# Kernel optimization log

Hardware: AMD Instinct MI355X
Metric: run time of the kernel (lower is better)

## Reference

```python
import jax, jax.numpy as jnp
import numpy as np

TOP_K = 2  # num_experts_per_tok


def setup_inputs() -> dict:
    key = jax.random.key(0)
    ks = jax.random.split(key, 5)
    B, T, D, E, F = 2, 2048, 1024, 8, 2048
    scale_d = 1.0 / np.sqrt(D)
    scale_f = 1.0 / np.sqrt(F)
    return {
        "x": jax.random.normal(ks[0], (B, T, D), jnp.float32),
        "kernel_router_DE": jax.random.normal(ks[1], (D, E), jnp.float32) * scale_d,
        "kernel_gating_EDF": jax.random.normal(ks[2], (E, D, F), jnp.float32) * scale_d,
        "kernel_up_EDF": jax.random.normal(ks[3], (E, D, F), jnp.float32) * scale_d,
        "kernel_down_EFD": jax.random.normal(ks[4], (E, F, D), jnp.float32) * scale_f,
    }


def reference(x, kernel_router_DE, kernel_gating_EDF, kernel_up_EDF, kernel_down_EFD):
    E = kernel_router_DE.shape[-1]
    x = x.astype(jnp.float32)

    # --- Router: logits -> softmax -> top_k -> renormalize with softmax ---
    router_logits_BTE = jnp.einsum('BTD,DE->BTE', x, kernel_router_DE)
    probs_BTE = jax.nn.softmax(router_logits_BTE.astype(jnp.float32), axis=-1)
    weights_BTX, indices_BTX = jax.lax.top_k(probs_BTE, TOP_K)
    norm_weights_BTX = jax.nn.softmax(weights_BTX, axis=-1)

    # --- Scatter top-k weights back to dense per-expert weights ---
    one_hot_BTXE = jax.nn.one_hot(indices_BTX, num_classes=E, dtype=jnp.float32)
    full_weights_BTE = jnp.sum(one_hot_BTXE * norm_weights_BTX[..., None], axis=2)

    # --- Dense all-expert MLP (gating * up -> down), weighted combine ---
    gating_BTEF = jnp.einsum('BTD,EDF->BTEF', x, kernel_gating_EDF)
    fuse_BTEF = jax.nn.silu(gating_BTEF) * jnp.einsum('BTD,EDF->BTEF', x, kernel_up_EDF)
    down_BTED = jnp.einsum('BTEF,EFD->BTED', fuse_BTEF, kernel_down_EFD)
    out_BTD = jnp.einsum('BTED,BTE->BTD', down_BTED, full_weights_BTE)
    return out_BTD.astype(jnp.float32)
```

## Files before the change

### kernel.cpp

```cpp
#include <hip/hip_runtime.h>
#include <cstdint>

#define N_TOK 4096
#define DIM   1024
#define NEXP  8
#define FDIM  2048

typedef _Float16 f16_t;
typedef _Float16 f16x8 __attribute__((ext_vector_type(8)));
typedef float    f32x4 __attribute__((ext_vector_type(4)));

__device__ inline unsigned packh(float a, float b) {
    union { f16_t h[2]; unsigned u; } p;
    p.h[0] = (f16_t)a; p.h[1] = (f16_t)b;
    return p.u;
}

__device__ inline void gl2lds16(const void* g, void* l) {
    __builtin_amdgcn_global_load_lds(
        (const __attribute__((address_space(1))) unsigned*)g,
        (__attribute__((address_space(3))) unsigned*)l, 16, 0, 0);
}

template<int N>
__device__ inline void vmw() {
    asm volatile("s_waitcnt vmcnt(%0)" :: "i"(N) : "memory");
}

__global__ __launch_bounds__(256) void router_kernel(
    const float* __restrict__ x, const float* __restrict__ wr,
    float* __restrict__ topw, int* __restrict__ counts, int* __restrict__ bucket)
{
    __shared__ float r[NEXP][DIM];
    __shared__ int sIdx[32];
    int tid = threadIdx.x;
    for (int i = tid; i < DIM * NEXP / 4; i += 256) {
        float4 v = ((const float4*)wr)[i];
        int base = i * 4;
        r[(base + 0) & 7][(base + 0) >> 3] = v.x;
        r[(base + 1) & 7][(base + 1) >> 3] = v.y;
        r[(base + 2) & 7][(base + 2) >> 3] = v.z;
        r[(base + 3) & 7][(base + 3) >> 3] = v.w;
    }
    __syncthreads();
    int wave = tid >> 6, lane = tid & 63;
    int t0 = blockIdx.x * 16 + wave * 4;
    for (int tt = 0; tt < 4; ++tt) {
        int t = t0 + tt;
        float acc[NEXP];
#pragma unroll
        for (int e = 0; e < NEXP; e++) acc[e] = 0.f;
        const float* xr = x + (size_t)t * DIM;
#pragma unroll
        for (int k = 0; k < DIM / 64; k++) {
            int d = lane + k * 64;
            float xv = xr[d];
#pragma unroll
            for (int e = 0; e < NEXP; e++) acc[e] += xv * r[e][d];
        }
#pragma unroll
        for (int e = 0; e < NEXP; e++) {
#pragma unroll
            for (int off = 32; off > 0; off >>= 1)
                acc[e] += __shfl_xor(acc[e], off, 64);
        }
        if (lane == 0) {
            float mx = acc[0];
#pragma unroll
            for (int e = 1; e < NEXP; e++) mx = fmaxf(mx, acc[e]);
            float p[NEXP]; float s = 0.f;
#pragma unroll
            for (int e = 0; e < NEXP; e++) { p[e] = expf(acc[e] - mx); s += p[e]; }
            float inv = 1.f / s;
#pragma unroll
            for (int e = 0; e < NEXP; e++) p[e] *= inv;
            int i1 = 0; float p1 = p[0];
#pragma unroll
            for (int e = 1; e < NEXP; e++) if (p[e] > p1) { p1 = p[e]; i1 = e; }
            int i2 = -1; float p2 = -1.f;
#pragma unroll
            for (int e = 0; e < NEXP; e++) if (e != i1 && p[e] > p2) { p2 = p[e]; i2 = e; }
            float e2 = expf(p2 - p1);
            float w1 = 1.f / (1.f + e2);
            topw[t * 2 + 0] = w1;
            topw[t * 2 + 1] = e2 * w1;
            int j = (wave * 4 + tt) * 2;
            sIdx[j + 0] = i1;
            sIdx[j + 1] = i2;
        }
    }
    __syncthreads();
    if (tid < NEXP) {
        int cnt = 0;
#pragma unroll
        for (int j = 0; j < 32; j++) cnt += (sIdx[j] == tid) ? 1 : 0;
        if (cnt > 0) {
            int pos = atomicAdd(&counts[tid * 32], cnt);
#pragma unroll
            for (int j = 0; j < 32; j++)
                if (sIdx[j] == tid)
                    bucket[tid * N_TOK + pos++] = (blockIdx.x * 16 + (j >> 1)) * 2 + (j & 1);
        }
    }
}

__global__ __launch_bounds__(256) void xcast_kernel(const float* __restrict__ x, f16_t* __restrict__ xf)
{
    int i = blockIdx.x * 256 + threadIdx.x;
    float4 a = ((const float4*)x)[2 * i];
    float4 b = ((const float4*)x)[2 * i + 1];
    union { f16_t h[8]; uint4 u; } p;
    p.h[0] = (f16_t)a.x; p.h[1] = (f16_t)a.y; p.h[2] = (f16_t)a.z; p.h[3] = (f16_t)a.w;
    p.h[4] = (f16_t)b.x; p.h[5] = (f16_t)b.y; p.h[6] = (f16_t)b.z; p.h[7] = (f16_t)b.w;
    ((uint4*)xf)[i] = p.u;
}

__global__ __launch_bounds__(256) void transpose_cvt(
    const float* __restrict__ inA, const float* __restrict__ inB,
    f16_t* __restrict__ outA, f16_t* __restrict__ outB,
    int R, int C, int tiles_r, int nA)
{
    __shared__ unsigned sP[64][68];
    int m = blockIdx.y;
    const float* in; f16_t* out;
    if (m < nA) { in = inA + (size_t)m * DIM * FDIM; out = outA + (size_t)m * DIM * FDIM; }
    else        { in = inB + (size_t)(m - nA) * DIM * FDIM; out = outB + (size_t)(m - nA) * DIM * FDIM; }
    int tix = blockIdx.x;
    int rb = (tix % tiles_r) * 128;
    int cb = (tix / tiles_r) * 64;
    int t = threadIdx.x;
    int dp = t >> 2;
    int fc = (t & 3) * 16;
    const float* r0 = in + (size_t)(rb + 2 * dp) * C + cb + fc;
    const float* r1 = r0 + C;
#pragma unroll
    for (int j = 0; j < 16; j += 4) {
        float4 a = *(const float4*)(r0 + j);
        float4 b = *(const float4*)(r1 + j);
        sP[fc + j + 0][dp] = packh(a.x, b.x);
        sP[fc + j + 1][dp] = packh(a.y, b.y);
        sP[fc + j + 2][dp] = packh(a.z, b.z);
        sP[fc + j + 3][dp] = packh(a.w, b.w);
    }
    __syncthreads();
    int c = t >> 2;
    int rc = t & 3;
    uint4* dst = (uint4*)(out + (size_t)(cb + c) * R + rb + rc * 32);
    const unsigned* src = &sP[c][rc * 16];
#pragma unroll
    for (int j = 0; j < 4; j++)
        dst[j] = *(const uint4*)(src + j * 4);
}

#define STG_A(NB, SLOT, KO)                                                     \
    gl2lds16(srcA0 + (KO), &lds[(NB)*32768 + (SLOT)*8192 + tid*8]);             \
    gl2lds16(srcA1 + (KO), &lds[(NB)*32768 + (SLOT)*8192 + 4096 + tid*8])
#define STG_B(NB, SLOT, KO)                                                     \
    gl2lds16(srcB0 + (KO), &lds[(NB)*32768 + (SLOT)*8192 + tid*8]);             \
    gl2lds16(srcB1 + (KO), &lds[(NB)*32768 + (SLOT)*8192 + 4096 + tid*8])

#define PHASE(KS, NH, VM, STAGE_STMT)                                           \
    {                                                                           \
        STAGE_STMT;                                                             \
        vmw<VM>();                                                              \
        __builtin_amdgcn_s_barrier();                                           \
        if ((NH) == 0) {                                                        \
            _Pragma("unroll")                                                   \
            for (int mi = 0; mi < 8; mi++)                                      \
                a[mi] = *(const f16x8*)&lds[bofs + ((KS)?2:0)*8192 +            \
                         (wr*128 + mi*16 + fm)*32 + p8];                        \
        }                                                                       \
        bb0 = *(const f16x8*)&lds[bofs + ((KS)?3:1)*8192 +                      \
               (wc*64 + ((NH)*2+0)*16 + fm)*32 + p8];                           \
        bb1 = *(const f16x8*)&lds[bofs + ((KS)?3:1)*8192 +                      \
               (wc*64 + ((NH)*2+1)*16 + fm)*32 + p8];                           \
        __builtin_amdgcn_s_setprio(1);                                          \
        _Pragma("unroll")                                                       \
        for (int mi = 0; mi < 8; mi++) {                                        \
            acc[mi][(NH)*2+0] = __builtin_amdgcn_mfma_f32_16x16x32_f16(         \
                a[mi], bb0, acc[mi][(NH)*2+0], 0, 0, 0);                        \
            acc[mi][(NH)*2+1] = __builtin_amdgcn_mfma_f32_16x16x32_f16(         \
                a[mi], bb1, acc[mi][(NH)*2+1], 0, 0, 0);                        \
        }                                                                       \
        __builtin_amdgcn_s_setprio(0);                                          \
        __builtin_amdgcn_s_barrier();                                           \
    }

__global__ __launch_bounds__(512) void gateup_kernel(
    const f16_t* __restrict__ xf,
    const f16_t* __restrict__ wgT, const f16_t* __restrict__ wuT,
    const int* __restrict__ counts, const int* __restrict__ bucket,
    f16_t* __restrict__ H)
{
    int flat = blockIdx.x + (blockIdx.y << 4) + (blockIdx.z << 8);
    int chunk = ((flat & 7) << 8) | (flat >> 3);
    int e  = chunk >> 8;
    int rr = chunk & 255;
    int m0 = (rr & 15) * 256;
    int f0 = (rr >> 4) * 128;
    int cnt = counts[e * 32];
    if (m0 >= cnt) return;

    __shared__ f16_t lds[2 * 4 * 8192];
    __shared__ int sEnt[256];

    int tid = threadIdx.x;
    if (tid < 256) {
        int i = m0 + tid;
        sEnt[tid] = bucket[e * N_TOK + (i < cnt ? i : m0)];
    }
    __syncthreads();

    int wave = tid >> 6, lane = tid & 63;
    int wr = wave >> 2, wc = wave & 3;
    int fm = lane & 15, quad = lane >> 4;
    int p8 = ((quad + (fm >> 1)) & 3) * 8;

    int row0 = tid >> 2;
    int row1 = 128 + row0;
    int c0 = ((tid & 3) - (row0 >> 1)) & 3;
    int c1 = ((tid & 3) - (row1 >> 1)) & 3;
    const f16_t* srcA0 = xf + (size_t)(sEnt[row0] >> 1) * DIM + c0 * 8;
    const f16_t* srcA1 = xf + (size_t)(sEnt[row1] >> 1) * DIM + c1 * 8;
    int wc4_0 = row0 >> 6, sub0 = row0 & 63;
    int wc4_1 = row1 >> 6, sub1 = row1 & 63;
    const f16_t* srcB0 = ((sub0 & 32) ? wuT : wgT) +
        ((size_t)e * FDIM + f0 + wc4_0 * 32 + (sub0 & 31)) * DIM + c0 * 8;
    const f16_t* srcB1 = ((sub1 & 32) ? wuT : wgT) +
        ((size_t)e * FDIM + f0 + wc4_1 * 32 + (sub1 & 31)) * DIM + c1 * 8;

    f32x4 acc[8][4];
    f32x4 zero = {0.f, 0.f, 0.f, 0.f};
#pragma unroll
    for (int i = 0; i < 8; i++)
#pragma unroll
        for (int j = 0; j < 4; j++) acc[i][j] = zero;

    f16x8 a[8], bb0, bb1;

    STG_A(0, 0, 0);
    STG_B(0, 1, 0);
    STG_A(0, 2, 32);
    STG_B(0, 3, 32);
    vmw<0>();
    __builtin_amdgcn_s_barrier();

    const int NT = DIM / 64;
    int b = 0;
    for (int t = 0; t < NT - 1; ++t) {
        int nb = b ^ 1;
        int bofs = b * 32768;
        int ko = (t + 1) * 64;
        PHASE(0, 0, 6, STG_A(nb, 0, ko));
        PHASE(0, 1, 6, STG_B(nb, 1, ko));
        PHASE(1, 0, 6, STG_A(nb, 2, ko + 32));
        PHASE(1, 1, 6, STG_B(nb, 3, ko + 32));
        b = nb;
    }
    {
        int bofs = b * 32768;
        PHASE(0, 0, 4, );
        PHASE(0, 1, 4, );
        PHASE(1, 0, 2, );
        PHASE(1, 1, 0, );
    }

    int crow = quad * 4;
#pragma unroll
    for (int mi = 0; mi < 8; mi++) {
#pragma unroll
        for (int i = 0; i < 4; i++) {
            int row = wr * 128 + mi * 16 + crow + i;
            if (m0 + row < cnt) {
                int ent = sEnt[row];
                f16_t* hr = H + (size_t)ent * FDIM + f0 + wc * 32;
#pragma unroll
                for (int ni = 0; ni < 2; ni++) {
                    float g = acc[mi][ni][i];
                    float u = acc[mi][ni + 2][i];
                    float h = (g / (1.f + __expf(-g))) * u;
                    hr[ni * 16 + fm] = (f16_t)h;
                }
            }
        }
    }
}

__global__ __launch_bounds__(256) void down_kernel(
    const f16_t* __restrict__ H, const f16_t* __restrict__ wdT,
    const int* __restrict__ counts, const int* __restrict__ bucket,
    const float* __restrict__ topw, float* __restrict__ Y)
{
    int e = blockIdx.z;
    int cnt = counts[e * 32];
    int m0 = blockIdx.y * 128;
    if (m0 >= cnt) return;
    int n0 = blockIdx.x * 128;

    __shared__ f16_t sA[128 * 32];
    __shared__ f16_t sB[128 * 32];
    __shared__ int sEnt[128];

    int tid = threadIdx.x;
    if (tid < 128) {
        int i = m0 + tid;
        sEnt[tid] = bucket[e * N_TOK + (i < cnt ? i : m0)];
    }
    __syncthreads();

    int wave = tid >> 6, lane = tid & 63;
    int q = ((lane & 3) - (lane >> 3)) & 3;
    int r0 = wave * 32 + (lane >> 2);
    int r1 = r0 + 16;
    const f16_t* gA0 = H + (size_t)sEnt[r0] * FDIM + q * 8;
    const f16_t* gA1 = H + (size_t)sEnt[r1] * FDIM + q * 8;
    const f16_t* gB0 = wdT + ((size_t)e * DIM + n0 + r0) * FDIM + q * 8;
    const f16_t* gB1 = wdT + ((size_t)e * DIM + n0 + r1) * FDIM + q * 8;
    f16_t* lA0 = &sA[wave * 1024 + lane * 8];
    f16_t* lA1 = lA0 + 512;
    f16_t* lB0 = &sB[wave * 1024 + lane * 8];
    f16_t* lB1 = lB0 + 512;

    f32x4 acc[4][4];
    f32x4 zero = {0.f, 0.f, 0.f, 0.f};
#pragma unroll
    for (int i = 0; i < 4; i++)
#pragma unroll
        for (int j = 0; j < 4; j++) acc[i][j] = zero;

    int wm = (wave & 1) * 64, wn = (wave >> 1) * 64;
    int fm = lane & 15, quad = lane >> 4;
    int p8 = ((quad + (fm >> 1)) & 3) * 8;

    for (int k0 = 0; k0 < FDIM; k0 += 32) {
        gl2lds16(gA0 + k0, lA0);
        gl2lds16(gA1 + k0, lA1);
        gl2lds16(gB0 + k0, lB0);
        gl2lds16(gB1 + k0, lB1);
        __syncthreads();
        f16x8 af[4], bf[4];
#pragma unroll
        for (int mi = 0; mi < 4; mi++)
            af[mi] = *(const f16x8*)&sA[(wm + mi * 16 + fm) * 32 + p8];
#pragma unroll
        for (int ni = 0; ni < 4; ni++)
            bf[ni] = *(const f16x8*)&sB[(wn + ni * 16 + fm) * 32 + p8];
#pragma unroll
        for (int mi = 0; mi < 4; mi++)
#pragma unroll
            for (int ni = 0; ni < 4; ni++)
                acc[mi][ni] = __builtin_amdgcn_mfma_f32_16x16x32_f16(af[mi], bf[ni], acc[mi][ni], 0, 0, 0);
        __syncthreads();
    }
    int crow = quad * 4, ccol = fm;
#pragma unroll
    for (int mi = 0; mi < 4; mi++) {
#pragma unroll
        for (int i = 0; i < 4; i++) {
            int m = wm + mi * 16 + crow + i;
            if (m0 + m < cnt) {
                int ent = sEnt[m];
                float w = topw[ent];
                float* yr = Y + (size_t)ent * DIM + n0 + wn;
#pragma unroll
                for (int ni = 0; ni < 4; ni++)
                    yr[ni * 16 + ccol] = w * acc[mi][ni][i];
            }
        }
    }
}

__global__ __launch_bounds__(256) void combine_kernel(
    const float* __restrict__ Y, float* __restrict__ out)
{
    int i = blockIdx.x * 256 + threadIdx.x;
    int t = i >> 8;
    int c = i & 255;
    float4 a = ((const float4*)Y)[(size_t)(2 * t) * 256 + c];
    float4 b = ((const float4*)Y)[(size_t)(2 * t + 1) * 256 + c];
    float4 o;
    o.x = a.x + b.x; o.y = a.y + b.y; o.z = a.z + b.z; o.w = a.w + b.w;
    ((float4*)out)[i] = o;
}

extern "C" void kernel_launch(void* const* d_in, const int* in_sizes, int n_in,
                              void* d_out, int out_size, void* d_ws, size_t ws_size,
                              hipStream_t stream) {
    const float* x  = (const float*)d_in[0];
    const float* wr = (const float*)d_in[1];
    const float* wg = (const float*)d_in[2];
    const float* wu = (const float*)d_in[3];
    const float* wd = (const float*)d_in[4];
    float* out = (float*)d_out;
    char* ws = (char*)d_ws;
    const size_t MB = 1ull << 20;

    int*   counts = (int*)ws;
    int*   bucket = (int*)(ws + 1024);
    float* topw   = (float*)(ws + 160 * 1024);
    f16_t* xf     = (f16_t*)(ws + 1 * MB);
    f16_t* wgT    = (f16_t*)(ws + 9 * MB);
    f16_t* wuT    = (f16_t*)(ws + 41 * MB);
    f16_t* H      = (f16_t*)(ws + 73 * MB);
    f16_t* wdT    = (f16_t*)(ws + 1 * MB);
    float* Y      = (float*)(ws + 33 * MB);

    hipMemsetAsync(counts, 0, 1024, stream);
    router_kernel<<<256, 256, 0, stream>>>(x, wr, topw, counts, bucket);
    xcast_kernel<<<2048, 256, 0, stream>>>(x, xf);
    transpose_cvt<<<dim3(256, 16), 256, 0, stream>>>(wg, wu, wgT, wuT, DIM, FDIM, DIM / 128, NEXP);
    gateup_kernel<<<dim3(16, 16, 8), 512, 0, stream>>>(xf, wgT, wuT, counts, bucket, H);
    transpose_cvt<<<dim3(256, 8), 256, 0, stream>>>(wd, wd, wdT, wdT, FDIM, DIM, FDIM / 128, NEXP);
    down_kernel<<<dim3(DIM / 128, 32, NEXP), 256, 0, stream>>>(H, wdT, counts, bucket, topw, Y);
    combine_kernel<<<4096, 256, 0, stream>>>(Y, out);
}
```

Baseline: 463.9 us.

## Switch gate/up GEMM to 4-slot ring buffer with one barrier per phase

Replaces the double-buffered 64-wide K pipeline with a 4-slot ring of 32-wide K stages, prefetching three stages ahead. LDS fragment reads for the current stage are issued before the next stage's global-to-LDS copies and the barrier, and the trailing barrier in each phase is removed. The aim is deeper latency hiding and less synchronisation. The risk is reduced correctness margin on slot reuse, since the slot being refilled must not still be read by lagging waves.

Result: faster. 432.9 us (-6.7%).

```diff
diff --git a/kernel.cpp b/kernel.cpp
--- a/kernel.cpp
+++ b/kernel.cpp
@@ -152,38 +152,37 @@
         dst[j] = *(const uint4*)(src + j * 4);
 }
 
-#define STG_A(NB, SLOT, KO)                                                     \
-    gl2lds16(srcA0 + (KO), &lds[(NB)*32768 + (SLOT)*8192 + tid*8]);             \
-    gl2lds16(srcA1 + (KO), &lds[(NB)*32768 + (SLOT)*8192 + 4096 + tid*8])
-#define STG_B(NB, SLOT, KO)                                                     \
-    gl2lds16(srcB0 + (KO), &lds[(NB)*32768 + (SLOT)*8192 + tid*8]);             \
-    gl2lds16(srcB1 + (KO), &lds[(NB)*32768 + (SLOT)*8192 + 4096 + tid*8])
-
-#define PHASE(KS, NH, VM, STAGE_STMT)                                           \
+#define STG_A(BOFS, KO)                                                         \
+    gl2lds16(srcA0 + (KO), &lds[(BOFS) + tid * 8]);                             \
+    gl2lds16(srcA1 + (KO), &lds[(BOFS) + 4096 + tid * 8])
+#define STG_B(BOFS, KO)                                                         \
+    gl2lds16(srcB0 + (KO), &lds[(BOFS) + 8192 + tid * 8]);                      \
+    gl2lds16(srcB1 + (KO), &lds[(BOFS) + 8192 + 4096 + tid * 8])
+
+#define PHASE(RB, NH, VM, STAGE_STMT)                                           \
     {                                                                           \
+        if ((NH) == 0) {                                                        \
+            _Pragma("unroll")                                                   \
+            for (int mi = 0; mi < 8; mi++)                                      \
+                a[mi] = *(const f16x8*)&lds[(RB) +                              \
+                         (wr * 128 + mi * 16 + fm) * 32 + p8];                  \
+        }                                                                       \
+        bb0 = *(const f16x8*)&lds[(RB) + 8192 +                                 \
+               (wc * 64 + ((NH) * 2 + 0) * 16 + fm) * 32 + p8];                 \
+        bb1 = *(const f16x8*)&lds[(RB) + 8192 +                                 \
+               (wc * 64 + ((NH) * 2 + 1) * 16 + fm) * 32 + p8];                 \
         STAGE_STMT;                                                             \
         vmw<VM>();                                                              \
         __builtin_amdgcn_s_barrier();                                           \
-        if ((NH) == 0) {                                                        \
-            _Pragma("unroll")                                                   \
-            for (int mi = 0; mi < 8; mi++)                                      \
-                a[mi] = *(const f16x8*)&lds[bofs + ((KS)?2:0)*8192 +            \
-                         (wr*128 + mi*16 + fm)*32 + p8];                        \
-        }                                                                       \
-        bb0 = *(const f16x8*)&lds[bofs + ((KS)?3:1)*8192 +                      \
-               (wc*64 + ((NH)*2+0)*16 + fm)*32 + p8];                           \
-        bb1 = *(const f16x8*)&lds[bofs + ((KS)?3:1)*8192 +                      \
-               (wc*64 + ((NH)*2+1)*16 + fm)*32 + p8];                           \
         __builtin_amdgcn_s_setprio(1);                                          \
         _Pragma("unroll")                                                       \
         for (int mi = 0; mi < 8; mi++) {                                        \
-            acc[mi][(NH)*2+0] = __builtin_amdgcn_mfma_f32_16x16x32_f16(         \
-                a[mi], bb0, acc[mi][(NH)*2+0], 0, 0, 0);                        \
-            acc[mi][(NH)*2+1] = __builtin_amdgcn_mfma_f32_16x16x32_f16(         \
-                a[mi], bb1, acc[mi][(NH)*2+1], 0, 0, 0);                        \
+            acc[mi][(NH) * 2 + 0] = __builtin_amdgcn_mfma_f32_16x16x32_f16(     \
+                a[mi], bb0, acc[mi][(NH) * 2 + 0], 0, 0, 0);                    \
+            acc[mi][(NH) * 2 + 1] = __builtin_amdgcn_mfma_f32_16x16x32_f16(     \
+                a[mi], bb1, acc[mi][(NH) * 2 + 1], 0, 0, 0);                    \
         }                                                                       \
         __builtin_amdgcn_s_setprio(0);                                          \
-        __builtin_amdgcn_s_barrier();                                           \
     }
 
 __global__ __launch_bounds__(512) void gateup_kernel(
@@ -201,7 +200,7 @@
     int cnt = counts[e * 32];
     if (m0 >= cnt) return;
 
-    __shared__ f16_t lds[2 * 4 * 8192];
+    __shared__ f16_t lds[4 * 16384];
     __shared__ int sEnt[256];
 
     int tid = threadIdx.x;
@@ -238,32 +237,29 @@
 
     f16x8 a[8], bb0, bb1;
 
-    STG_A(0, 0, 0);
-    STG_B(0, 1, 0);
-    STG_A(0, 2, 32);
-    STG_B(0, 3, 32);
-    vmw<0>();
+    STG_A(0, 0);      STG_B(0, 0);
+    STG_A(16384, 32); STG_B(16384, 32);
+    STG_A(32768, 64); STG_B(32768, 64);
+    vmw<8>();
     __builtin_amdgcn_s_barrier();
 
-    const int NT = DIM / 64;
-    int b = 0;
-    for (int t = 0; t < NT - 1; ++t) {
-        int nb = b ^ 1;
-        int bofs = b * 32768;
-        int ko = (t + 1) * 64;
-        PHASE(0, 0, 6, STG_A(nb, 0, ko));
-        PHASE(0, 1, 6, STG_B(nb, 1, ko));
-        PHASE(1, 0, 6, STG_A(nb, 2, ko + 32));
-        PHASE(1, 1, 6, STG_B(nb, 3, ko + 32));
-        b = nb;
-    }
-    {
-        int bofs = b * 32768;
-        PHASE(0, 0, 4, );
-        PHASE(0, 1, 4, );
-        PHASE(1, 0, 2, );
-        PHASE(1, 1, 0, );
-    }
+    const int NT = DIM / 32;
+    int rb = 0;
+    for (int t = 0; t < NT - 3; ++t) {
+        int sb = (rb + 49152) & 65535;
+        int ko = (t + 3) * 32;
+        PHASE(rb, 0, 8, STG_A(sb, ko));
+        PHASE(rb, 1, 8, STG_B(sb, ko));
+        rb = (rb + 16384) & 65535;
+    }
+    PHASE(rb, 0, 8, );
+    PHASE(rb, 1, 4, );
+    rb = (rb + 16384) & 65535;
+    PHASE(rb, 0, 4, );
+    PHASE(rb, 1, 0, );
+    rb = (rb + 16384) & 65535;
+    PHASE(rb, 0, 0, );
+    PHASE(rb, 1, 0, );
 
     int crow = quad * 4;
 #pragma unroll
```
